# Kernel optimization log

Measured on AMD Instinct MI355X. Metric: run time of the kernel, lower is better.

The kernel has to match this reference:

```python
import jax, jax.numpy as jnp
from jax import lax
import numpy as np

HEADS, SAMPLES = 4, 8
B, C, D, H, W = 1, 64, 16, 64, 64
HD = C // HEADS  # head_dim = 16
BN_EPS = 1e-5


def conv3d(x, w, b=None, pad=0):
    out = lax.conv_general_dilated(
        x, w, (1, 1, 1), [(pad, pad)] * 3,
        dimension_numbers=("NCDHW", "OIDHW", "NCDHW"))
    if b is not None:
        out = out + b[None, :, None, None, None]
    return out


def trilinear_sample(vol, grid):
    # vol: [Dv,Hv,Wv,Cc]; grid: [...,3] with torch grid_sample semantics:
    # grid[...,0] -> x (W axis), grid[...,1] -> y (H axis), grid[...,2] -> z (D axis)
    # align_corners=True, padding_mode='border'. Returns [..., Cc].
    Dv, Hv, Wv, _ = vol.shape
    ix = (grid[..., 0] + 1.0) * 0.5 * (Wv - 1)
    iy = (grid[..., 1] + 1.0) * 0.5 * (Hv - 1)
    iz = (grid[..., 2] + 1.0) * 0.5 * (Dv - 1)
    x0 = jnp.floor(ix); y0 = jnp.floor(iy); z0 = jnp.floor(iz)
    wx = (ix - x0)[..., None]; wy = (iy - y0)[..., None]; wz = (iz - z0)[..., None]
    x0i = jnp.clip(x0.astype(jnp.int32), 0, Wv - 1); x1i = jnp.clip(x0i + 1, 0, Wv - 1)
    y0i = jnp.clip(y0.astype(jnp.int32), 0, Hv - 1); y1i = jnp.clip(y0i + 1, 0, Hv - 1)
    z0i = jnp.clip(z0.astype(jnp.int32), 0, Dv - 1); z1i = jnp.clip(z0i + 1, 0, Dv - 1)
    g = lambda z, y, x: vol[z, y, x]
    out = (g(z0i, y0i, x0i) * (1 - wz) * (1 - wy) * (1 - wx)
           + g(z0i, y0i, x1i) * (1 - wz) * (1 - wy) * wx
           + g(z0i, y1i, x0i) * (1 - wz) * wy * (1 - wx)
           + g(z0i, y1i, x1i) * (1 - wz) * wy * wx
           + g(z1i, y0i, x0i) * wz * (1 - wy) * (1 - wx)
           + g(z1i, y0i, x1i) * wz * (1 - wy) * wx
           + g(z1i, y1i, x0i) * wz * wy * (1 - wx)
           + g(z1i, y1i, x1i) * wz * wy * wx)
    return out


def t_deform(feat_prev, feat_curr, p):
    b, c, d, h, w = feat_curr.shape
    kv = conv3d(feat_prev, p["kv_w"], p["kv_b"])          # [B,2C,D,H,W]
    q = conv3d(feat_curr, p["q_w"], p["q_b"])              # [B,C,D,H,W]
    # offset branch: conv3x3 -> GELU(exact) -> conv3x3(no bias) -> tanh
    o = conv3d(feat_curr, p["off1_w"], p["off1_b"], pad=1)
    o = jax.nn.gelu(o, approximate=False)
    o = jnp.tanh(conv3d(o, p["off2_w"], None, pad=1))      # [B,M*S*3,D,H,W]
    off = o.reshape(b, HEADS, SAMPLES, 3, d, h, w).transpose(0, 1, 4, 5, 6, 2, 3)  # [B,M,D,H,W,S,3]
    zz, yy, xx = jnp.meshgrid(jnp.linspace(-1, 1, d), jnp.linspace(-1, 1, h),
                              jnp.linspace(-1, 1, w), indexing="ij")
    base = jnp.stack((zz, yy, xx), axis=-1).astype(feat_curr.dtype)  # [D,H,W,3]
    scale = jnp.array([d, h, w], dtype=feat_curr.dtype)
    grid = base[None, None, :, :, :, None, :] + off / scale
    grid = jnp.clip(grid, -1.0, 1.0)
    grid = grid.transpose(0, 1, 5, 2, 3, 4, 6).reshape(b * HEADS, SAMPLES, d, h, w, 3)
    # channels-last per (batch,head) volume; avoids torch's explicit repeat over samples
    vols = kv.reshape(b, HEADS, 2 * HD, d, h, w).transpose(0, 1, 3, 4, 5, 2)
    vols = vols.reshape(b * HEADS, d, h, w, 2 * HD)
    sampled = jax.vmap(trilinear_sample)(vols, grid)        # [B*M,S,D,H,W,2*HD]
    sampled = sampled.reshape(b, HEADS, SAMPLES, d, h, w, 2 * HD)
    key, value = sampled[..., :HD], sampled[..., HD:]
    qh = q.reshape(b, HEADS, HD, d, h, w) * (HD ** -0.5)
    attn = jnp.einsum("bmcdhw,bmsdhwc->bmsdhw", qh, key)
    attn = jax.nn.softmax(attn, axis=2)
    fused = jnp.einsum("bmsdhw,bmsdhwc->bmcdhw", attn, value).reshape(b, c, d, h, w)
    out = conv3d(fused, p["out_w"], p["out_b"])
    # BatchNorm3d (eval: running stats) + ReLU
    inv = lax.rsqrt(p["bn_var"] + BN_EPS)
    out = (out - p["bn_mean"][None, :, None, None, None]) * (inv * p["bn_gamma"])[None, :, None, None, None] \
          + p["bn_beta"][None, :, None, None, None]
    return jax.nn.relu(out)


def setup_inputs() -> dict:
    key = jax.random.key(0)
    ks = jax.random.split(key, 16)
    r = lambda k, shp, s=0.05: (jax.random.normal(k, shp, dtype=jnp.float32) * s)
    return {
        "mid_feat": jax.random.normal(ks[0], (B, C, D, H, W), dtype=jnp.float32),
        "occ_feat": jax.random.normal(ks[1], (B, C, D, H, W), dtype=jnp.float32),
        "prev_feat": jax.random.normal(ks[2], (B, C, D, H, W), dtype=jnp.float32),
        "off1_w": r(ks[3], (C, C, 3, 3, 3)), "off1_b": r(ks[4], (C,)),
        "off2_w": r(ks[5], (HEADS * SAMPLES * 3, C, 3, 3, 3)),
        "kv_w": r(ks[6], (2 * C, C, 1, 1, 1)), "kv_b": r(ks[7], (2 * C,)),
        "q_w": r(ks[8], (C, C, 1, 1, 1)), "q_b": r(ks[9], (C,)),
        "out_w": r(ks[10], (C, C, 1, 1, 1)), "out_b": r(ks[11], (C,)),
        "bn_gamma": jnp.ones((C,), jnp.float32), "bn_beta": jnp.zeros((C,), jnp.float32),
        "bn_mean": jnp.zeros((C,), jnp.float32), "bn_var": jnp.ones((C,), jnp.float32),
    }


def reference(mid_feat, occ_feat, prev_feat, off1_w, off1_b, off2_w, kv_w, kv_b,
              q_w, q_b, out_w, out_b, bn_gamma, bn_beta, bn_mean, bn_var):
    p = dict(off1_w=off1_w, off1_b=off1_b, off2_w=off2_w, kv_w=kv_w, kv_b=kv_b,
             q_w=q_w, q_b=q_b, out_w=out_w, out_b=out_b, bn_gamma=bn_gamma,
             bn_beta=bn_beta, bn_mean=bn_mean, bn_var=bn_var)
    d1 = t_deform(mid_feat, occ_feat, p)
    d2 = t_deform(mid_feat, prev_feat, p)
    return jnp.concatenate([mid_feat, d1, d2], axis=1)  # [B,3C,D,H,W]
```

## Files before the change

kernel.cpp:

```cpp
#include <hip/hip_runtime.h>
#include <math.h>

#define DD 16
#define HH 64
#define WW 64
#define VV (DD*HH*WW)
#define CC 64
#define NHEADS 4
#define NSAMP 8
#define HDIM 16

typedef unsigned int uint;
typedef unsigned short ushort;
typedef __attribute__((ext_vector_type(8))) short bf16x8;
typedef __attribute__((ext_vector_type(4))) float f32x4;

__device__ __forceinline__ float clampf(float v, float lo, float hi){ return fminf(fmaxf(v, lo), hi); }
__device__ __forceinline__ int imin(int a, int b){ return a < b ? a : b; }

__device__ __forceinline__ ushort f2bf(float f){
  uint u = __float_as_uint(f);
  uint r = (u + 0x7fffu + ((u>>16)&1u)) >> 16;
  return (ushort)r;
}
__device__ __forceinline__ uint packbf2(float a, float b){
  return (uint)f2bf(a) | ((uint)f2bf(b) << 16);
}
__device__ __forceinline__ float bflo(uint u){ return __uint_as_float(u << 16); }
__device__ __forceinline__ float bfhi(uint u){ return __uint_as_float(u & 0xffff0000u); }
__device__ __forceinline__ float bf2f(ushort u){ return __uint_as_float((uint)u << 16); }

__device__ __forceinline__ float fast_tanh(float x){
  float e = __expf(2.f*x);
  return 1.f - 2.f/(e + 1.f);
}

__device__ __forceinline__ void repack_wmfma_body(const float* __restrict__ w,
                                                  uint* __restrict__ o, int MG, int U){
  int j2 = U & 3;
  int m  = (U>>2) & 15;
  int q  = (U>>6) & 3;
  int rest = U >> 8;
  int g = rest % MG;
  int s = rest / MG;
  int tap = s >> 1, h = s & 1;
  int co = g*16 + m;
  int ci = h*32 + q*8 + j2*2;
  int base = co*1728 + ci*27 + tap;
  o[U] = packbf2(w[base], w[base + 27]);
}
__device__ __forceinline__ void repack_w1_body(const float* __restrict__ w,
                                               uint* __restrict__ o, int MT, int U){
  int j2 = U & 3;
  int lane = (U>>2) & 63;
  int frag = U >> 8;
  int mt = frag % MT;
  int ks = frag / MT;
  int q = lane >> 4, m = lane & 15;
  int co = mt*16 + m;
  int ci = ks*32 + q*8 + j2*2;
  o[U] = packbf2(w[co*CC + ci], w[co*CC + ci + 1]);
}

__global__ __launch_bounds__(256) void prep(
    const float* __restrict__ occ, const float* __restrict__ prev,
    uint* __restrict__ o0pk,
    const float* __restrict__ off1w, uint* __restrict__ wA1,
    const float* __restrict__ off2w, uint* __restrict__ wA2,
    const float* __restrict__ outw, uint* __restrict__ wo,
    const float* __restrict__ kvw,  uint* __restrict__ wkv,
    const float* __restrict__ qw,   uint* __restrict__ wq)
{
  int b = blockIdx.x, tid = threadIdx.x;
  if (b < 2048){
    int idx = b*256 + tid;
    int v4 = (idx & (VV/4 - 1)) * 4;
    int rest = idx >> 14;
    int cq = rest & 15;
    int call = rest >> 4;
    const float* x = call ? prev : occ;
    const float* p0 = x + (size_t)(cq*4)*VV + v4;
    float4 f0 = *reinterpret_cast<const float4*>(p0);
    float4 f1 = *reinterpret_cast<const float4*>(p0 + VV);
    float4 f2 = *reinterpret_cast<const float4*>(p0 + 2*VV);
    float4 f3 = *reinterpret_cast<const float4*>(p0 + 3*VV);
    uint* ob = o0pk + ((size_t)(call*16 + cq)*VV + v4)*2;
    uint4 w0, w1;
    w0.x = packbf2(f0.x, f1.x); w0.y = packbf2(f2.x, f3.x);
    w0.z = packbf2(f0.y, f1.y); w0.w = packbf2(f2.y, f3.y);
    w1.x = packbf2(f0.z, f1.z); w1.y = packbf2(f2.z, f3.z);
    w1.z = packbf2(f0.w, f1.w); w1.w = packbf2(f2.w, f3.w);
    *reinterpret_cast<uint4*>(ob)     = w0;
    *reinterpret_cast<uint4*>(ob + 4) = w1;
  }
  else if (b < 2264){ repack_wmfma_body(off1w, wA1, 4, (b-2048)*256 + tid); }
  else if (b < 2588){ repack_wmfma_body(off2w, wA2, 6, (b-2264)*256 + tid); }
  else if (b < 2596){ repack_w1_body(outw, wo, 4, (b-2588)*256 + tid); }
  else if (b < 2612){ repack_w1_body(kvw, wkv, 8, (b-2596)*256 + tid); }
  else              { repack_w1_body(qw,  wq, 4, (b-2612)*256 + tid); }
}

template<int CO, int EPI>
__global__ __launch_bounds__(256) void conv1_mfma(
    const float* __restrict__ xf, const uint* __restrict__ xq,
    const uint* __restrict__ wA, const float* __restrict__ bias,
    void* __restrict__ outp, float* __restrict__ mcopy)
{
  constexpr int MT = CO/16;
  constexpr int MW = MT/4;
  __shared__ ushort xt[64*72];
  int tid = threadIdx.x;
  int lane = tid & 63;
  int g = __builtin_amdgcn_readfirstlane(tid >> 6);
  int q = lane >> 4, n = lane & 15;
  int call = blockIdx.x >> 10;
  int v0 = (blockIdx.x & 1023) * 64;
  if constexpr (EPI == 0){
    for (int it = tid; it < 64*32; it += 256){
      int vox = it & 63; int cp = it >> 6;
      float a = xf[(size_t)(2*cp)*VV + v0 + vox];
      float b = xf[(size_t)(2*cp+1)*VV + v0 + vox];
      mcopy[(size_t)(2*cp)*VV + v0 + vox] = a;
      mcopy[(size_t)(2*cp+1)*VV + v0 + vox] = b;
      *reinterpret_cast<uint*>(&xt[vox*72 + 2*cp]) = packbf2(a,b);
    }
  } else {
    const uint2* xp = reinterpret_cast<const uint2*>(xq) + (size_t)call*16*VV;
    for (int it = tid; it < 64*16; it += 256){
      int vox = it & 63; int cq = it >> 6;
      *reinterpret_cast<uint2*>(&xt[vox*72 + cq*4]) = xp[(size_t)cq*VV + v0 + vox];
    }
  }
  __syncthreads();
  f32x4 acc[MW][4];
  #pragma unroll
  for (int mw=0;mw<MW;mw++)
    #pragma unroll
    for (int nt=0;nt<4;nt++){ acc[mw][nt].x=0.f; acc[mw][nt].y=0.f; acc[mw][nt].z=0.f; acc[mw][nt].w=0.f; }
  const char* ldsb = reinterpret_cast<const char*>(xt);
  const char* wac  = reinterpret_cast<const char*>(wA);
  #pragma unroll
  for (int ks=0; ks<2; ks++){
    bf16x8 bfr[4];
    #pragma unroll
    for (int nt=0; nt<4; nt++)
      bfr[nt] = *reinterpret_cast<const bf16x8*>(ldsb + ((nt*16+n)*144 + q*16 + ks*64));
    #pragma unroll
    for (int mw=0; mw<MW; mw++){
      int mt = g*MW + mw;
      bf16x8 af = *reinterpret_cast<const bf16x8*>(wac + (size_t)((ks*MT + mt)*64 + lane)*16);
      #pragma unroll
      for (int nt=0; nt<4; nt++)
        acc[mw][nt] = __builtin_amdgcn_mfma_f32_16x16x32_bf16(af, bfr[nt], acc[mw][nt], 0, 0, 0);
    }
  }
  if constexpr (EPI == 0){
    #pragma unroll
    for (int mw=0; mw<MW; mw++){
      int mt = g*MW + mw;
      int cob = mt*16 + q*4;
      #pragma unroll
      for (int nt=0; nt<4; nt++){
        int v = v0 + nt*16 + n;
        float r0 = acc[mw][nt].x + bias[cob+0];
        float r1 = acc[mw][nt].y + bias[cob+1];
        float r2 = acc[mw][nt].z + bias[cob+2];
        float r3 = acc[mw][nt].w + bias[cob+3];
        int z = v >> 12, y = (v >> 6) & 63, xx = v & 63;
        int head = cob >> 5;
        uint* vols = (uint*)outp;
        uint2 pk; pk.x = packbf2(r0,r1); pk.y = packbf2(r2,r3);
        *reinterpret_cast<uint2*>(vols + ((size_t)head*VV + (size_t)(y*WW+xx)*DD + z)*16 + ((cob&31)>>1)) = pk;
      }
    }
  } else {
    __syncthreads();
    ushort* xr = xt;
    int cob = g*16 + q*4;
    #pragma unroll
    for (int nt=0; nt<4; nt++){
      int vox = nt*16 + n;
      uint2 pk;
      pk.x = packbf2((acc[0][nt].x + bias[cob+0])*0.25f, (acc[0][nt].y + bias[cob+1])*0.25f);
      pk.y = packbf2((acc[0][nt].z + bias[cob+2])*0.25f, (acc[0][nt].w + bias[cob+3])*0.25f);
      *reinterpret_cast<uint2*>(&xr[vox*64 + cob]) = pk;
    }
    __syncthreads();
    char* ob = (char*)((ushort*)outp + (size_t)call*CC*VV) + (size_t)v0*128;
    const char* lb = reinterpret_cast<const char*>(xr);
    #pragma unroll
    for (int k=0; k<2; k++){
      int idx = tid + k*256;
      *reinterpret_cast<uint4*>(ob + idx*16) = *reinterpret_cast<const uint4*>(lb + idx*16);
    }
  }
}

template<int CO, int OUTPK>
__global__ __launch_bounds__(256) void conv3_mfma(
    const uint* __restrict__ xpk,
    const uint* __restrict__ wA, const float* __restrict__ bias,
    void* __restrict__ outp)
{
  constexpr int MG = CO/16;
  constexpr int MROW = CO/32;
  __shared__ ushort xh[24576];
  int tid = threadIdx.x;
  int lane = tid & 63;
  int w = __builtin_amdgcn_readfirstlane(tid >> 6);
  int q = lane >> 4, n = lane & 15;
  int bid = blockIdx.x;
  int xcd = bid & 7, islot = bid >> 3;
  int call = xcd >> 2;
  int z0 = (xcd & 3) * 4;
  int by = (islot >> 3) << 3, bx = (islot & 7) << 3;

  const uint2* xinp = reinterpret_cast<const uint2*>(xpk) + (size_t)call*16*VV;

  int mbase = (w & 1) * MROW;
  int nzh = (w >> 1) * 2;
  int lo[8];
  #pragma unroll
  for (int nt=0;nt<8;nt++){
    int zi = nzh + (nt>>2);
    int vl = (nt&3)*16 + n;
    lo[nt] = (zi*100 + (vl>>3)*10 + (vl&7))*80 + q*16;
  }
  f32x4 acc[MROW][8];
  #pragma unroll
  for (int mr=0;mr<MROW;mr++)
    #pragma unroll
    for (int nt=0;nt<8;nt++){ acc[mr][nt].x=0.f; acc[mr][nt].y=0.f; acc[mr][nt].z=0.f; acc[mr][nt].w=0.f; }

  const char* ldsb = reinterpret_cast<const char*>(xh);
  const char* wac  = reinterpret_cast<const char*>(wA);

  uint2 pq[19];
  auto load_half = [&](int h){
    #pragma unroll
    for (int k=0;k<19;k++){
      int it = tid + k*256;
      if (it < 4800){
        int cg = it/600; int pos = it - cg*600;
        int dz = pos/100; int rr = pos - dz*100; int dy = rr/10; int dxx = rr - dy*10;
        int gz = z0 + dz - 1, gy = by + dy - 1, gx = bx + dxx - 1;
        uint2 v; v.x = 0u; v.y = 0u;
        if (gz>=0 && gz<DD && gy>=0 && gy<HH && gx>=0 && gx<WW)
          v = xinp[(size_t)(h*8+cg)*VV + (size_t)((gz*HH+gy)*WW + gx)];
        pq[k] = v;
      }
    }
  };
  auto write_half = [&](){
    #pragma unroll
    for (int k=0;k<19;k++){
      int it = tid + k*256;
      if (it < 4800){
        int cg = it/600; int pos = it - cg*600;
        *reinterpret_cast<uint2*>(&xh[pos*40 + cg*4]) = pq[k];
      }
    }
  };
  auto compute_half = [&](int h){
    #pragma unroll 2
    for (int tap=0; tap<27; tap++){
      int dz = tap/9; int r9 = tap - dz*9; int dy = r9/3; int dxx = r9 - dy*3;
      int stepOff = (dz*100 + dy*10 + dxx)*80;
      int s = tap*2 + h;
      bf16x8 af[MROW];
      #pragma unroll
      for (int mr=0;mr<MROW;mr++)
        af[mr] = *reinterpret_cast<const bf16x8*>(wac + (size_t)((s*MG + mbase+mr)*64 + lane)*16);
      bf16x8 bf[8];
      #pragma unroll
      for (int nt=0;nt<8;nt++)
        bf[nt] = *reinterpret_cast<const bf16x8*>(ldsb + (lo[nt] + stepOff));
      #pragma unroll
      for (int mr=0;mr<MROW;mr++)
        #pragma unroll
        for (int nt=0;nt<8;nt++)
          acc[mr][nt] = __builtin_amdgcn_mfma_f32_16x16x32_bf16(af[mr], bf[nt], acc[mr][nt], 0, 0, 0);
    }
  };

  load_half(0);
  write_half();
  __syncthreads();
  load_half(1);
  compute_half(0);
  __syncthreads();
  write_half();
  __syncthreads();
  compute_half(1);

  if (OUTPK == 1){
    #pragma unroll
    for (int mr=0; mr<MROW; mr++){
      int cob = (mbase+mr)*16 + q*4;
      #pragma unroll
      for (int nt=0; nt<8; nt++){
        int zi = nzh + (nt>>2);
        int vl = (nt&3)*16 + n;
        int vy = by + (vl>>3), vx = bx + (vl&7);
        size_t gv = (size_t)(((z0+zi)*HH + vy)*WW + vx);
        float r0 = acc[mr][nt].x + bias[cob+0];
        float r1 = acc[mr][nt].y + bias[cob+1];
        float r2 = acc[mr][nt].z + bias[cob+2];
        float r3 = acc[mr][nt].w + bias[cob+3];
        r0 = 0.5f*r0*(1.f + erff(r0*0.70710678118654752f));
        r1 = 0.5f*r1*(1.f + erff(r1*0.70710678118654752f));
        r2 = 0.5f*r2*(1.f + erff(r2*0.70710678118654752f));
        r3 = 0.5f*r3*(1.f + erff(r3*0.70710678118654752f));
        uint2 pk; pk.x = packbf2(r0,r1); pk.y = packbf2(r2,r3);
        uint* dst = (uint*)outp;
        *reinterpret_cast<uint2*>(dst + ((size_t)(call*16 + (cob>>2))*VV + gv)*2) = pk;
      }
    }
  } else {
    __syncthreads();
    ushort* xr = xh;
    #pragma unroll
    for (int mr=0; mr<MROW; mr++){
      int cob = (mbase+mr)*16 + q*4;
      #pragma unroll
      for (int nt=0; nt<8; nt++){
        int row = (nzh + (nt>>2))*64 + (nt&3)*16 + n;
        uint2 pk;
        pk.x = packbf2(fast_tanh(acc[mr][nt].x), fast_tanh(acc[mr][nt].y));
        pk.y = packbf2(fast_tanh(acc[mr][nt].z), fast_tanh(acc[mr][nt].w));
        *reinterpret_cast<uint2*>(&xr[row*96 + cob]) = pk;
      }
    }
    __syncthreads();
    ushort* dst = (ushort*)outp + (size_t)call*96*VV;
    const char* lb = reinterpret_cast<const char*>(xr);
    #pragma unroll
    for (int k=0; k<12; k++){
      int idx = tid + k*256;
      int chunk = idx/96;
      int off = idx - chunk*96;
      int zi = chunk>>3, y8 = chunk&7;
      size_t gb = (size_t)(((z0+zi)*HH + by + y8)*WW + bx)*192 + (size_t)off*16;
      *reinterpret_cast<uint4*>((char*)dst + gb) = *reinterpret_cast<const uint4*>(lb + idx*16);
    }
  }
}

struct Geom { int x0,x1,y0,y1,z0,z1; float wx,wy,wz; };
__device__ __forceinline__ Geom make_geom(float zb, float yb, float xb,
                                          float o0, float o1, float o2){
  float g0 = clampf(zb + o0*(1.f/16.f), -1.f, 1.f);
  float g1 = clampf(yb + o1*(1.f/64.f), -1.f, 1.f);
  float g2 = clampf(xb + o2*(1.f/64.f), -1.f, 1.f);
  float ix = (g0+1.f)*0.5f*63.f;
  float iy = (g1+1.f)*0.5f*63.f;
  float iz = (g2+1.f)*0.5f*15.f;
  float fx=floorf(ix), fy=floorf(iy), fz=floorf(iz);
  Geom g;
  g.wx = ix-fx; g.wy = iy-fy; g.wz = iz-fz;
  g.x0 = (int)fx; g.x1 = imin(g.x0+1, WW-1);
  g.y0 = (int)fy; g.y1 = imin(g.y0+1, HH-1);
  g.z0 = (int)fz; g.z1 = imin(g.z0+1, DD-1);
  return g;
}

__global__ __launch_bounds__(256) void sample_attn_kernel(
    const ushort* __restrict__ qbuf, const ushort* __restrict__ offbuf,
    const uint* __restrict__ vols, const uint* __restrict__ woA,
    const float* __restrict__ outb, const float* __restrict__ bng,
    const float* __restrict__ bnb, const float* __restrict__ bnm,
    const float* __restrict__ bnv, float* __restrict__ dout)
{
  __shared__ ushort fsb[16*72];
  int t = threadIdx.x;
  int lane = t & 63;
  int m = __builtin_amdgcn_readfirstlane(t >> 6);
  int slot = lane >> 2;
  int r = lane & 3;
  int bid = blockIdx.x;
  int xcd = bid & 7, islot = bid >> 3;
  int call = islot >> 9;
  int z = xcd*2 + ((islot >> 8) & 1);
  int rem = islot & 255;
  int y = rem >> 2;
  int x0 = (rem & 3) << 4;
  int x = x0 + slot;
  int vbase = (z*HH + y)*WW + x0;
  int v = vbase + slot;

  const ushort* qb = qbuf   + (size_t)call*CC*VV;
  const ushort* ob = offbuf + (size_t)call*96*VV;

  uint4 qu = *reinterpret_cast<const uint4*>(qb + (size_t)v*64 + m*16 + (r&1)*8);
  float qf[8];
  qf[0]=bflo(qu.x); qf[1]=bfhi(qu.x); qf[2]=bflo(qu.y); qf[3]=bfhi(qu.y);
  qf[4]=bflo(qu.z); qf[5]=bfhi(qu.z); qf[6]=bflo(qu.w); qf[7]=bfhi(qu.w);

  uint ou[12];
  {
    const uint4* op4 = reinterpret_cast<const uint4*>(ob + (size_t)v*96 + m*24);
    uint4 a = op4[0], b4 = op4[1], c4 = op4[2];
    ou[0]=a.x;  ou[1]=a.y;  ou[2]=a.z;  ou[3]=a.w;
    ou[4]=b4.x; ou[5]=b4.y; ou[6]=b4.z; ou[7]=b4.w;
    ou[8]=c4.x; ou[9]=c4.y; ou[10]=c4.z; ou[11]=c4.w;
  }

  float zbf = -1.f + (float)z*(2.f/15.f);
  float ybf = -1.f + (float)y*(2.f/63.f);
  float xbf = -1.f + (float)x*(2.f/63.f);

  const char* volb = reinterpret_cast<const char*>(vols) + (size_t)m*VV*64;
  float roleK = (r < 2) ? 1.f : 0.f;
  float lrun = 0.f;
  float fused[8];
  #pragma unroll
  for (int c=0;c<8;c++) fused[c]=0.f;

  #pragma unroll
  for (int s=0;s<NSAMP;s++){
    int i0 = 3*s, i1 = 3*s+1, i2 = 3*s+2;
    float o0 = (i0&1) ? bfhi(ou[i0>>1]) : bflo(ou[i0>>1]);
    float o1 = (i1&1) ? bfhi(ou[i1>>1]) : bflo(ou[i1>>1]);
    float o2 = (i2&1) ? bfhi(ou[i2>>1]) : bflo(ou[i2>>1]);
    Geom g = make_geom(zbf,ybf,xbf,o0,o1,o2);
    int tz0 = g.z0*64 + r*16;
    int tz1 = g.z1*64 + r*16;
    float wx1 = g.wx, wx0 = 1.f-g.wx;
    float wy1 = g.wy, wy0 = 1.f-g.wy;
    float wz1 = g.wz, wz0 = 1.f-g.wz;
    float acc[8];
    #pragma unroll
    for (int c=0;c<8;c++) acc[c]=0.f;
    #pragma unroll
    for (int ky=0;ky<2;ky++)
    #pragma unroll
    for (int kx=0;kx<2;kx++){
      int cy = ky? g.y1:g.y0, cx = kx? g.x1:g.x0;
      float wyx = (ky? wy1:wy0)*(kx? wx1:wx0);
      float a0 = wyx*wz0, a1 = wyx*wz1;
      uint wzp;
      asm("v_cvt_pk_bf16_f32 %0, %1, %2" : "=v"(wzp) : "v"(a0), "v"(a1));
      int tb = ((cy<<6) + cx) << 10;
      const char* p = volb + tb;
      uint4 u0 = *reinterpret_cast<const uint4*>(p + tz0);
      uint4 u1 = *reinterpret_cast<const uint4*>(p + tz1);
      uint plo, phi;
      plo = __builtin_amdgcn_perm(u1.x, u0.x, 0x05040100u);
      phi = __builtin_amdgcn_perm(u1.x, u0.x, 0x07060302u);
      asm("v_dot2_f32_bf16 %0, %1, %2, %0" : "+v"(acc[0]) : "v"(plo), "v"(wzp));
      asm("v_dot2_f32_bf16 %0, %1, %2, %0" : "+v"(acc[1]) : "v"(phi), "v"(wzp));
      plo = __builtin_amdgcn_perm(u1.y, u0.y, 0x05040100u);
      phi = __builtin_amdgcn_perm(u1.y, u0.y, 0x07060302u);
      asm("v_dot2_f32_bf16 %0, %1, %2, %0" : "+v"(acc[2]) : "v"(plo), "v"(wzp));
      asm("v_dot2_f32_bf16 %0, %1, %2, %0" : "+v"(acc[3]) : "v"(phi), "v"(wzp));
      plo = __builtin_amdgcn_perm(u1.z, u0.z, 0x05040100u);
      phi = __builtin_amdgcn_perm(u1.z, u0.z, 0x07060302u);
      asm("v_dot2_f32_bf16 %0, %1, %2, %0" : "+v"(acc[4]) : "v"(plo), "v"(wzp));
      asm("v_dot2_f32_bf16 %0, %1, %2, %0" : "+v"(acc[5]) : "v"(phi), "v"(wzp));
      plo = __builtin_amdgcn_perm(u1.w, u0.w, 0x05040100u);
      phi = __builtin_amdgcn_perm(u1.w, u0.w, 0x07060302u);
      asm("v_dot2_f32_bf16 %0, %1, %2, %0" : "+v"(acc[6]) : "v"(plo), "v"(wzp));
      asm("v_dot2_f32_bf16 %0, %1, %2, %0" : "+v"(acc[7]) : "v"(phi), "v"(wzp));
    }
    float h = qf[0]*acc[0]+qf[1]*acc[1]+qf[2]*acc[2]+qf[3]*acc[3]
            + qf[4]*acc[4]+qf[5]*acc[5]+qf[6]*acc[6]+qf[7]*acc[7];
    h *= roleK;
    h += __shfl_xor(h, 1);
    h += __shfl_xor(h, 2);
    float e = __expf(h);
    lrun += e;
    #pragma unroll
    for (int c=0;c<8;c++) fused[c] += e*acc[c];
  }
  float isum = 1.f/lrun;
  if (r >= 2){
    uint4 pk;
    pk.x = packbf2(fused[0]*isum, fused[1]*isum);
    pk.y = packbf2(fused[2]*isum, fused[3]*isum);
    pk.z = packbf2(fused[4]*isum, fused[5]*isum);
    pk.w = packbf2(fused[6]*isum, fused[7]*isum);
    *reinterpret_cast<uint4*>(&fsb[slot*72 + m*16 + (r&1)*8]) = pk;
  }
  __syncthreads();

  int qq = lane >> 4, n = lane & 15;
  f32x4 acco;
  acco.x=0.f; acco.y=0.f; acco.z=0.f; acco.w=0.f;
  const char* ldsb = reinterpret_cast<const char*>(fsb);
  const char* wac  = reinterpret_cast<const char*>(woA);
  #pragma unroll
  for (int ks=0; ks<2; ks++){
    bf16x8 af = *reinterpret_cast<const bf16x8*>(wac + (size_t)((ks*4 + m)*64 + lane)*16);
    bf16x8 bfv = *reinterpret_cast<const bf16x8*>(ldsb + (n*144 + qq*16 + ks*64));
    acco = __builtin_amdgcn_mfma_f32_16x16x32_bf16(af, bfv, acco, 0, 0, 0);
  }
  int choff = 64 + call*64;
  #pragma unroll
  for (int rr=0; rr<4; rr++){
    int co = m*16 + qq*4 + rr;
    float inv = rsqrtf(bnv[co] + 1e-5f) * bng[co];
    float val = (acco[rr] + outb[co] - bnm[co]) * inv + bnb[co];
    val = fmaxf(val, 0.f);
    dout[(size_t)(choff+co)*VV + vbase + n] = val;
  }
}

extern "C" void kernel_launch(void* const* d_in, const int* in_sizes, int n_in,
                              void* d_out, int out_size, void* d_ws, size_t ws_size,
                              hipStream_t stream){
  (void)in_sizes; (void)n_in; (void)out_size; (void)ws_size;
  const float* mid  = (const float*)d_in[0];
  const float* occ  = (const float*)d_in[1];
  const float* prev = (const float*)d_in[2];
  const float* off1w= (const float*)d_in[3];
  const float* off1b= (const float*)d_in[4];
  const float* off2w= (const float*)d_in[5];
  const float* kvw  = (const float*)d_in[6];
  const float* kvb  = (const float*)d_in[7];
  const float* qw   = (const float*)d_in[8];
  const float* qb   = (const float*)d_in[9];
  const float* outw = (const float*)d_in[10];
  const float* outb = (const float*)d_in[11];
  const float* bng  = (const float*)d_in[12];
  const float* bnb  = (const float*)d_in[13];
  const float* bnm  = (const float*)d_in[14];
  const float* bnv  = (const float*)d_in[15];
  float* out = (float*)d_out;

  uint*   vols  = (uint*)d_ws;
  ushort* qbuf  = (ushort*)(vols + (size_t)4*VV*16);
  uint*   o1pk  = (uint*)(qbuf + (size_t)2*CC*VV);
  ushort* offb  = (ushort*)(o1pk + (size_t)2*32*VV);
  uint*   wA1   = (uint*)(offb + (size_t)2*96*VV);
  uint*   wA2   = wA1 + 55296;
  uint*   wo    = wA2 + 82944;
  uint*   wkv   = wo  + 2048;
  uint*   wq    = wkv + 4096;
  uint*   o0pk  = wq  + 2048;

  prep<<<2620, 256, 0, stream>>>(occ, prev, o0pk, off1w, wA1, off2w, wA2,
                                 outw, wo, kvw, wkv, qw, wq);
  conv1_mfma<128,0><<<1024, 256, 0, stream>>>(mid, nullptr, wkv, kvb, (void*)vols, out);
  conv1_mfma<64,1><<<2048, 256, 0, stream>>>(nullptr, o0pk, wq, qb, (void*)qbuf, nullptr);
  conv3_mfma<64,1><<<512, 256, 0, stream>>>(o0pk, wA1, off1b, (void*)o1pk);
  conv3_mfma<96,0><<<512, 256, 0, stream>>>(o1pk, wA2, off1b, (void*)offb);
  sample_attn_kernel<<<8192, 256, 0, stream>>>(qbuf, offb, vols, wo,
      outb, bng, bnb, bnm, bnv, out);
}
```

Before: 327.6 us.

## Fuse 1x1 convs into prep kernel and build weight fragments on the fly

Merges the prep kernel and both 1x1 conv kernels (kv and q projections) into a single fused_front launch. The q conv now reads fp32 occ/prev directly instead of waiting for the packed bf16 copy, and the small 1x1 weight matrices are converted to bf16 MFMA fragments in registers at use time rather than repacked into workspace. The second 3x3 conv drops its register prefetch double-buffering in favour of a simpler load-then-compute loop, likely to cut register pressure. This removes two launches and their serialization, at the cost of redundant weight conversion in every block and possibly lower occupancy for the fused kernel.

```diff
diff --git a/kernel.cpp b/kernel.cpp
--- a/kernel.cpp
+++ b/kernel.cpp
@@ -33,6 +33,16 @@
 __device__ __forceinline__ float fast_tanh(float x){
   float e = __expf(2.f*x);
   return 1.f - 2.f/(e + 1.f);
+}
+
+__device__ __forceinline__ bf16x8 make_af(const float* __restrict__ w, int mt, int ks, int lane){
+  const float* p = w + (size_t)(mt*16 + (lane&15))*CC + ks*32 + ((lane>>4)<<3);
+  float4 f0 = *reinterpret_cast<const float4*>(p);
+  float4 f1 = *reinterpret_cast<const float4*>(p+4);
+  union { uint4 u; bf16x8 b; } r;
+  r.u.x = packbf2(f0.x, f0.y); r.u.y = packbf2(f0.z, f0.w);
+  r.u.z = packbf2(f1.x, f1.y); r.u.w = packbf2(f1.z, f1.w);
+  return r.b;
 }
 
 __device__ __forceinline__ void repack_wmfma_body(const float* __restrict__ w,
@@ -49,27 +59,108 @@
   int base = co*1728 + ci*27 + tap;
   o[U] = packbf2(w[base], w[base + 27]);
 }
-__device__ __forceinline__ void repack_w1_body(const float* __restrict__ w,
-                                               uint* __restrict__ o, int MT, int U){
-  int j2 = U & 3;
-  int lane = (U>>2) & 63;
-  int frag = U >> 8;
-  int mt = frag % MT;
-  int ks = frag / MT;
-  int q = lane >> 4, m = lane & 15;
-  int co = mt*16 + m;
-  int ci = ks*32 + q*8 + j2*2;
-  o[U] = packbf2(w[co*CC + ci], w[co*CC + ci + 1]);
-}
-
-__global__ __launch_bounds__(256) void prep(
+
+template<int CO, int EPI>
+__device__ void conv1_body(
+    int bid, int tid,
+    const float* __restrict__ xa, const float* __restrict__ xb,
+    const float* __restrict__ wraw, const float* __restrict__ bias,
+    void* __restrict__ outp, float* __restrict__ mcopy)
+{
+  constexpr int MT = CO/16;
+  constexpr int MW = MT/4;
+  __shared__ ushort xt[64*72];
+  int lane = tid & 63;
+  int g = __builtin_amdgcn_readfirstlane(tid >> 6);
+  int q = lane >> 4, n = lane & 15;
+  int call = bid >> 10;
+  int v0 = (bid & 1023) * 64;
+  bf16x8 afr[2][MW];
+  #pragma unroll
+  for (int ks=0; ks<2; ks++)
+    #pragma unroll
+    for (int mw=0; mw<MW; mw++)
+      afr[ks][mw] = make_af(wraw, g*MW+mw, ks, lane);
+  const float* x = call ? xb : xa;
+  for (int it = tid; it < 64*32; it += 256){
+    int vox = it & 63; int cp = it >> 6;
+    float a = x[(size_t)(2*cp)*VV + v0 + vox];
+    float b = x[(size_t)(2*cp+1)*VV + v0 + vox];
+    if constexpr (EPI == 0){
+      mcopy[(size_t)(2*cp)*VV + v0 + vox] = a;
+      mcopy[(size_t)(2*cp+1)*VV + v0 + vox] = b;
+    }
+    *reinterpret_cast<uint*>(&xt[vox*72 + 2*cp]) = packbf2(a,b);
+  }
+  __syncthreads();
+  f32x4 acc[MW][4];
+  #pragma unroll
+  for (int mw=0;mw<MW;mw++)
+    #pragma unroll
+    for (int nt=0;nt<4;nt++){ acc[mw][nt].x=0.f; acc[mw][nt].y=0.f; acc[mw][nt].z=0.f; acc[mw][nt].w=0.f; }
+  const char* ldsb = reinterpret_cast<const char*>(xt);
+  #pragma unroll
+  for (int ks=0; ks<2; ks++){
+    bf16x8 bfr[4];
+    #pragma unroll
+    for (int nt=0; nt<4; nt++)
+      bfr[nt] = *reinterpret_cast<const bf16x8*>(ldsb + ((nt*16+n)*144 + q*16 + ks*64));
+    #pragma unroll
+    for (int mw=0; mw<MW; mw++)
+      #pragma unroll
+      for (int nt=0; nt<4; nt++)
+        acc[mw][nt] = __builtin_amdgcn_mfma_f32_16x16x32_bf16(afr[ks][mw], bfr[nt], acc[mw][nt], 0, 0, 0);
+  }
+  if constexpr (EPI == 0){
+    #pragma unroll
+    for (int mw=0; mw<MW; mw++){
+      int mt = g*MW + mw;
+      int cob = mt*16 + q*4;
+      #pragma unroll
+      for (int nt=0; nt<4; nt++){
+        int v = v0 + nt*16 + n;
+        float r0 = acc[mw][nt].x + bias[cob+0];
+        float r1 = acc[mw][nt].y + bias[cob+1];
+        float r2 = acc[mw][nt].z + bias[cob+2];
+        float r3 = acc[mw][nt].w + bias[cob+3];
+        int z = v >> 12, y = (v >> 6) & 63, xx = v & 63;
+        int head = cob >> 5;
+        uint* vols = (uint*)outp;
+        uint2 pk; pk.x = packbf2(r0,r1); pk.y = packbf2(r2,r3);
+        *reinterpret_cast<uint2*>(vols + ((size_t)head*VV + (size_t)(y*WW+xx)*DD + z)*16 + ((cob&31)>>1)) = pk;
+      }
+    }
+  } else {
+    __syncthreads();
+    ushort* xr = xt;
+    int cob = g*16 + q*4;
+    #pragma unroll
+    for (int nt=0; nt<4; nt++){
+      int vox = nt*16 + n;
+      uint2 pk;
+      pk.x = packbf2((acc[0][nt].x + bias[cob+0])*0.25f, (acc[0][nt].y + bias[cob+1])*0.25f);
+      pk.y = packbf2((acc[0][nt].z + bias[cob+2])*0.25f, (acc[0][nt].w + bias[cob+3])*0.25f);
+      *reinterpret_cast<uint2*>(&xr[vox*64 + cob]) = pk;
+    }
+    __syncthreads();
+    char* ob = (char*)((ushort*)outp + (size_t)call*CC*VV) + (size_t)v0*128;
+    const char* lb = reinterpret_cast<const char*>(xr);
+    #pragma unroll
+    for (int k=0; k<2; k++){
+      int idx = tid + k*256;
+      *reinterpret_cast<uint4*>(ob + idx*16) = *reinterpret_cast<const uint4*>(lb + idx*16);
+    }
+  }
+}
+
+__global__ __launch_bounds__(256) void fused_front(
     const float* __restrict__ occ, const float* __restrict__ prev,
-    uint* __restrict__ o0pk,
+    const float* __restrict__ mid, uint* __restrict__ o0pk,
     const float* __restrict__ off1w, uint* __restrict__ wA1,
     const float* __restrict__ off2w, uint* __restrict__ wA2,
-    const float* __restrict__ outw, uint* __restrict__ wo,
-    const float* __restrict__ kvw,  uint* __restrict__ wkv,
-    const float* __restrict__ qw,   uint* __restrict__ wq)
+    const float* __restrict__ kvw,  const float* __restrict__ kvb,
+    const float* __restrict__ qw,   const float* __restrict__ qb,
+    void* __restrict__ vols, void* __restrict__ qbuf, float* __restrict__ out)
 {
   int b = blockIdx.x, tid = threadIdx.x;
   if (b < 2048){
@@ -95,108 +186,11 @@
   }
   else if (b < 2264){ repack_wmfma_body(off1w, wA1, 4, (b-2048)*256 + tid); }
   else if (b < 2588){ repack_wmfma_body(off2w, wA2, 6, (b-2264)*256 + tid); }
-  else if (b < 2596){ repack_w1_body(outw, wo, 4, (b-2588)*256 + tid); }
-  else if (b < 2612){ repack_w1_body(kvw, wkv, 8, (b-2596)*256 + tid); }
-  else              { repack_w1_body(qw,  wq, 4, (b-2612)*256 + tid); }
-}
-
-template<int CO, int EPI>
-__global__ __launch_bounds__(256) void conv1_mfma(
-    const float* __restrict__ xf, const uint* __restrict__ xq,
-    const uint* __restrict__ wA, const float* __restrict__ bias,
-    void* __restrict__ outp, float* __restrict__ mcopy)
-{
-  constexpr int MT = CO/16;
-  constexpr int MW = MT/4;
-  __shared__ ushort xt[64*72];
-  int tid = threadIdx.x;
-  int lane = tid & 63;
-  int g = __builtin_amdgcn_readfirstlane(tid >> 6);
-  int q = lane >> 4, n = lane & 15;
-  int call = blockIdx.x >> 10;
-  int v0 = (blockIdx.x & 1023) * 64;
-  if constexpr (EPI == 0){
-    for (int it = tid; it < 64*32; it += 256){
-      int vox = it & 63; int cp = it >> 6;
-      float a = xf[(size_t)(2*cp)*VV + v0 + vox];
-      float b = xf[(size_t)(2*cp+1)*VV + v0 + vox];
-      mcopy[(size_t)(2*cp)*VV + v0 + vox] = a;
-      mcopy[(size_t)(2*cp+1)*VV + v0 + vox] = b;
-      *reinterpret_cast<uint*>(&xt[vox*72 + 2*cp]) = packbf2(a,b);
-    }
-  } else {
-    const uint2* xp = reinterpret_cast<const uint2*>(xq) + (size_t)call*16*VV;
-    for (int it = tid; it < 64*16; it += 256){
-      int vox = it & 63; int cq = it >> 6;
-      *reinterpret_cast<uint2*>(&xt[vox*72 + cq*4]) = xp[(size_t)cq*VV + v0 + vox];
-    }
-  }
-  __syncthreads();
-  f32x4 acc[MW][4];
-  #pragma unroll
-  for (int mw=0;mw<MW;mw++)
-    #pragma unroll
-    for (int nt=0;nt<4;nt++){ acc[mw][nt].x=0.f; acc[mw][nt].y=0.f; acc[mw][nt].z=0.f; acc[mw][nt].w=0.f; }
-  const char* ldsb = reinterpret_cast<const char*>(xt);
-  const char* wac  = reinterpret_cast<const char*>(wA);
-  #pragma unroll
-  for (int ks=0; ks<2; ks++){
-    bf16x8 bfr[4];
-    #pragma unroll
-    for (int nt=0; nt<4; nt++)
-      bfr[nt] = *reinterpret_cast<const bf16x8*>(ldsb + ((nt*16+n)*144 + q*16 + ks*64));
-    #pragma unroll
-    for (int mw=0; mw<MW; mw++){
-      int mt = g*MW + mw;
-      bf16x8 af = *reinterpret_cast<const bf16x8*>(wac + (size_t)((ks*MT + mt)*64 + lane)*16);
-      #pragma unroll
-      for (int nt=0; nt<4; nt++)
-        acc[mw][nt] = __builtin_amdgcn_mfma_f32_16x16x32_bf16(af, bfr[nt], acc[mw][nt], 0, 0, 0);
-    }
-  }
-  if constexpr (EPI == 0){
-    #pragma unroll
-    for (int mw=0; mw<MW; mw++){
-      int mt = g*MW + mw;
-      int cob = mt*16 + q*4;
-      #pragma unroll
-      for (int nt=0; nt<4; nt++){
-        int v = v0 + nt*16 + n;
-        float r0 = acc[mw][nt].x + bias[cob+0];
-        float r1 = acc[mw][nt].y + bias[cob+1];
-        float r2 = acc[mw][nt].z + bias[cob+2];
-        float r3 = acc[mw][nt].w + bias[cob+3];
-        int z = v >> 12, y = (v >> 6) & 63, xx = v & 63;
-        int head = cob >> 5;
-        uint* vols = (uint*)outp;
-        uint2 pk; pk.x = packbf2(r0,r1); pk.y = packbf2(r2,r3);
-        *reinterpret_cast<uint2*>(vols + ((size_t)head*VV + (size_t)(y*WW+xx)*DD + z)*16 + ((cob&31)>>1)) = pk;
-      }
-    }
-  } else {
-    __syncthreads();
-    ushort* xr = xt;
-    int cob = g*16 + q*4;
-    #pragma unroll
-    for (int nt=0; nt<4; nt++){
-      int vox = nt*16 + n;
-      uint2 pk;
-      pk.x = packbf2((acc[0][nt].x + bias[cob+0])*0.25f, (acc[0][nt].y + bias[cob+1])*0.25f);
-      pk.y = packbf2((acc[0][nt].z + bias[cob+2])*0.25f, (acc[0][nt].w + bias[cob+3])*0.25f);
-      *reinterpret_cast<uint2*>(&xr[vox*64 + cob]) = pk;
-    }
-    __syncthreads();
-    char* ob = (char*)((ushort*)outp + (size_t)call*CC*VV) + (size_t)v0*128;
-    const char* lb = reinterpret_cast<const char*>(xr);
-    #pragma unroll
-    for (int k=0; k<2; k++){
-      int idx = tid + k*256;
-      *reinterpret_cast<uint4*>(ob + idx*16) = *reinterpret_cast<const uint4*>(lb + idx*16);
-    }
-  }
-}
-
-template<int CO, int OUTPK>
+  else if (b < 3612){ conv1_body<128,0>(b-2588, tid, mid, nullptr, kvw, kvb, vols, out); }
+  else              { conv1_body<64,1>(b-3612, tid, occ, prev, qw, qb, qbuf, nullptr); }
+}
+
+template<int CO, int OUTPK, int PREF>
 __global__ __launch_bounds__(256) void conv3_mfma(
     const uint* __restrict__ xpk,
     const uint* __restrict__ wA, const float* __restrict__ bias,
@@ -235,32 +229,6 @@
   const char* ldsb = reinterpret_cast<const char*>(xh);
   const char* wac  = reinterpret_cast<const char*>(wA);
 
-  uint2 pq[19];
-  auto load_half = [&](int h){
-    #pragma unroll
-    for (int k=0;k<19;k++){
-      int it = tid + k*256;
-      if (it < 4800){
-        int cg = it/600; int pos = it - cg*600;
-        int dz = pos/100; int rr = pos - dz*100; int dy = rr/10; int dxx = rr - dy*10;
-        int gz = z0 + dz - 1, gy = by + dy - 1, gx = bx + dxx - 1;
-        uint2 v; v.x = 0u; v.y = 0u;
-        if (gz>=0 && gz<DD && gy>=0 && gy<HH && gx>=0 && gx<WW)
-          v = xinp[(size_t)(h*8+cg)*VV + (size_t)((gz*HH+gy)*WW + gx)];
-        pq[k] = v;
-      }
-    }
-  };
-  auto write_half = [&](){
-    #pragma unroll
-    for (int k=0;k<19;k++){
-      int it = tid + k*256;
-      if (it < 4800){
-        int cg = it/600; int pos = it - cg*600;
-        *reinterpret_cast<uint2*>(&xh[pos*40 + cg*4]) = pq[k];
-      }
-    }
-  };
   auto compute_half = [&](int h){
     #pragma unroll 2
     for (int tap=0; tap<27; tap++){
@@ -283,15 +251,62 @@
     }
   };
 
-  load_half(0);
-  write_half();
-  __syncthreads();
-  load_half(1);
-  compute_half(0);
-  __syncthreads();
-  write_half();
-  __syncthreads();
-  compute_half(1);
+  if constexpr (PREF){
+    uint2 pq[19];
+    auto load_half = [&](int h){
+      #pragma unroll
+      for (int k=0;k<19;k++){
+        int it = tid + k*256;
+        if (it < 4800){
+          int cg = it/600; int pos = it - cg*600;
+          int dz = pos/100; int rr = pos - dz*100; int dy = rr/10; int dxx = rr - dy*10;
+          int gz = z0 + dz - 1, gy = by + dy - 1, gx = bx + dxx - 1;
+          uint2 v; v.x = 0u; v.y = 0u;
+          if (gz>=0 && gz<DD && gy>=0 && gy<HH && gx>=0 && gx<WW)
+            v = xinp[(size_t)(h*8+cg)*VV + (size_t)((gz*HH+gy)*WW + gx)];
+          pq[k] = v;
+        }
+      }
+    };
+    auto write_half = [&](){
+      #pragma unroll
+      for (int k=0;k<19;k++){
+        int it = tid + k*256;
+        if (it < 4800){
+          int cg = it/600; int pos = it - cg*600;
+          *reinterpret_cast<uint2*>(&xh[pos*40 + cg*4]) = pq[k];
+        }
+      }
+    };
+    load_half(0);
+    write_half();
+    __syncthreads();
+    load_half(1);
+    compute_half(0);
+    __syncthreads();
+    write_half();
+    __syncthreads();
+    compute_half(1);
+  } else {
+    #pragma unroll 1
+    for (int h=0; h<2; h++){
+      if (h) __syncthreads();
+      for (int k=0;k<19;k++){
+        int it = tid + k*256;
+        if (it < 4800){
+          int cg = it/600; int pos = it - cg*600;
+          int dz = pos/100; int rr = pos - dz*100; int dy = rr/10; int dxx = rr - dy*10;
+          int gz = z0 + dz - 1, gy = by + dy - 1, gx = bx + dxx - 1;
+          uint2 v; v.x = 0u; v.y = 0u;
+          if (gz>=0 && gz<DD && gy>=0 && gy<HH && gx>=0 && gx<WW)
+            v = xinp[(size_t)(h*8+cg)*VV + (size_t)((gz*HH+gy)*WW + gx)];
+          *reinterpret_cast<uint2*>(&xh[pos*40 + cg*4]) = v;
+        }
+      }
+      __syncthreads();
+      compute_half(h);
+    }
+  }
 
   if (OUTPK == 1){
     #pragma unroll
@@ -366,7 +381,7 @@
 
 __global__ __launch_bounds__(256) void sample_attn_kernel(
     const ushort* __restrict__ qbuf, const ushort* __restrict__ offbuf,
-    const uint* __restrict__ vols, const uint* __restrict__ woA,
+    const uint* __restrict__ vols, const float* __restrict__ outw,
     const float* __restrict__ outb, const float* __restrict__ bng,
     const float* __restrict__ bnb, const float* __restrict__ bnm,
     const float* __restrict__ bnv, float* __restrict__ dout)
@@ -487,10 +502,9 @@
   f32x4 acco;
   acco.x=0.f; acco.y=0.f; acco.z=0.f; acco.w=0.f;
   const char* ldsb = reinterpret_cast<const char*>(fsb);
-  const char* wac  = reinterpret_cast<const char*>(woA);
   #pragma unroll
   for (int ks=0; ks<2; ks++){
-    bf16x8 af = *reinterpret_cast<const bf16x8*>(wac + (size_t)((ks*4 + m)*64 + lane)*16);
+    bf16x8 af = make_af(outw, m, ks, lane);
     bf16x8 bfv = *reinterpret_cast<const bf16x8*>(ldsb + (n*144 + qq*16 + ks*64));
     acco = __builtin_amdgcn_mfma_f32_16x16x32_bf16(af, bfv, acco, 0, 0, 0);
   }
@@ -533,17 +547,13 @@
   ushort* offb  = (ushort*)(o1pk + (size_t)2*32*VV);
   uint*   wA1   = (uint*)(offb + (size_t)2*96*VV);
   uint*   wA2   = wA1 + 55296;
-  uint*   wo    = wA2 + 82944;
-  uint*   wkv   = wo  + 2048;
-  uint*   wq    = wkv + 4096;
-  uint*   o0pk  = wq  + 2048;
-
-  prep<<<2620, 256, 0, stream>>>(occ, prev, o0pk, off1w, wA1, off2w, wA2,
-                                 outw, wo, kvw, wkv, qw, wq);
-  conv1_mfma<128,0><<<1024, 256, 0, stream>>>(mid, nullptr, wkv, kvb, (void*)vols, out);
-  conv1_mfma<64,1><<<2048, 256, 0, stream>>>(nullptr, o0pk, wq, qb, (void*)qbuf, nullptr);
-  conv3_mfma<64,1><<<512, 256, 0, stream>>>(o0pk, wA1, off1b, (void*)o1pk);
-  conv3_mfma<96,0><<<512, 256, 0, stream>>>(o1pk, wA2, off1b, (void*)offb);
-  sample_attn_kernel<<<8192, 256, 0, stream>>>(qbuf, offb, vols, wo,
+  uint*   o0pk  = wA2 + 82944;
+
+  fused_front<<<5660, 256, 0, stream>>>(occ, prev, mid, o0pk,
+      off1w, wA1, off2w, wA2, kvw, kvb, qw, qb,
+      (void*)vols, (void*)qbuf, out);
+  conv3_mfma<64,1,1><<<512, 256, 0, stream>>>(o0pk, wA1, off1b, (void*)o1pk);
+  conv3_mfma<96,0,0><<<512, 256, 0, stream>>>(o1pk, wA2, off1b, (void*)offb);
+  sample_attn_kernel<<<8192, 256, 0, stream>>>(qbuf, offb, vols, outw,
       outb, bng, bnb, bnm, bnv, out);
 }
```

Result: no change. 332.3 us (+1.4%).
